# Kernel tuning notes

Hardware: AMD Instinct MI355X
Metric: run time of the kernel (lower is better)

The kernel has to match this reference:

```python
import jax, jax.numpy as jnp
import numpy as np
from jax.ops import segment_sum, segment_max

ALPHA = 0.01  # leaky relu slope

def _cmul(a, b):
    # complex multiply on last-axis (re, im) pairs
    re = a[..., 0] * b[..., 0] - a[..., 1] * b[..., 1]
    im = a[..., 0] * b[..., 1] + a[..., 1] * b[..., 0]
    return jnp.stack((re, im), axis=-1)

def setup_inputs() -> dict:
    key = jax.random.key(0)
    ks = jax.random.split(key, 8)
    N, D, M, E, L, H, R, FH = 50000, 64, 3, 100000, 4, 8, 5, 128
    return {
        "features": jax.random.normal(ks[0], (N, D), jnp.float32),
        "attn1_w": jax.random.normal(ks[1], (M, H, D), jnp.float32) * 0.1,
        "attn2":   jax.random.normal(ks[2], (M, H, D), jnp.float32) * 0.1,
        "r_vec":   jax.random.normal(ks[3], (R, D // 2, 2), jnp.float32),
        "proj_w1": jax.random.normal(ks[4], (FH, H * D), jnp.float32) * 0.05,
        "proj_b1": jnp.zeros((FH,), jnp.float32),
        "proj_w2": jax.random.normal(ks[5], (1, FH), jnp.float32) * 0.1,
        "inst":    jax.random.randint(ks[6], (M, E, L), 0, N),
        "etypes":  jax.random.randint(ks[7], (M, L - 1), 0, 2 * R, dtype=jnp.int32),
    }

def reference(features, attn1_w, attn2, r_vec, proj_w1, proj_b1, proj_w2, inst, etypes):
    N, D = features.shape
    M, E, L = inst.shape
    H = attn1_w.shape[1]
    # --- conjugate-augmented, L2-normalized relation rotations ([2R, D/2, 2]) ---
    rn = r_vec / jnp.linalg.norm(r_vec, axis=2, keepdims=True)
    conj = rn * jnp.array([1.0, -1.0], rn.dtype)
    r_full = jnp.stack((rn, conj), axis=1).reshape(2 * r_vec.shape[0], r_vec.shape[1], 2)

    node_embs = []  # per-metapath [N, H*D]
    for m in range(M):
        # SemanticEncoder: gather + rotation recurrence + mean over path positions
        edata = features[inst[m]]                       # [E, L, D]
        edc = edata.reshape(E, L, D // 2, 2)
        # final_r_vec: backward cumulative complex product; position L-1 = identity
        ident = jnp.concatenate(
            [jnp.ones((D // 2, 1), edata.dtype), jnp.zeros((D // 2, 1), edata.dtype)], axis=-1)
        fr = [None] * L
        fr[L - 1] = ident
        for i in range(L - 2, -1, -1):
            fr[i] = _cmul(fr[i + 1], r_full[etypes[m, i]])
        fr = jnp.stack(fr, axis=0)                      # [L, D/2, 2]
        rotated = _cmul(edc, fr[None])                  # [E, L, D/2, 2] (pos L-1 rotated by identity)
        me = rotated.reshape(E, L, D).mean(axis=1)      # metapath embedding [E, D]

        # MessageAggregator: GAT-style segment softmax over instances per dst node
        dst = inst[m, :, 0]                             # [E]
        a1 = features[dst] @ attn1_w[m].T               # [E, H]
        a2 = jnp.einsum('ed,hd->eh', me, attn2[m])      # [E, H]
        a = jax.nn.leaky_relu(a1 + a2, ALPHA)           # [E, H]
        amax = segment_max(a, dst, num_segments=N)      # [N, H]
        amax = jnp.where(jnp.isfinite(amax), amax, 0.0)
        ex = jnp.exp(a - amax[dst])                     # [E, H]
        den = segment_sum(ex, dst, num_segments=N)      # [N, H]
        attn = ex / jnp.where(den[dst] > 0, den[dst], 1.0)
        agg = segment_sum(attn[:, :, None] * me[:, None, :], dst, num_segments=N)  # [N, H, D]
        node_embs.append(jax.nn.elu(agg).reshape(N, H * D))

    # Subgraph_Fusion: semantic attention over metapaths
    z = jnp.stack(node_embs, axis=1)                    # [N, M, H*D]
    w = jnp.tanh(z @ proj_w1.T + proj_b1) @ proj_w2.T   # [N, M, 1]
    beta = jax.nn.softmax(w.mean(axis=0), axis=0)       # [M, 1]
    out = (beta[None] * z).sum(axis=1)                  # [N, H*D]
    return out
```

## Files before the change

kernel.cpp:

```cpp
#include <hip/hip_runtime.h>
#include <hip/hip_bf16.h>
#include <math.h>

#define NN 50000
#define DD 64
#define MM 3
#define EE 100000
#define LL 4
#define HH 8
#define FHH 128
#define HD 512
#define NROWS (NN*MM)
#define LRELU_ALPHA 0.01f

#define WSUM_BINS 256
#define WSUM_SZ (MM*WSUM_BINS)
#define BINS (MM*NN)
#define NBLK ((BINS + 1023)/1024)
#define GT_TILE 224

#define OFF_ZB    0
#define OFF_WSUM  (NROWS*HD/2)
#define OFF_BETA  (OFF_WSUM + WSUM_SZ)
#define OFF_W1BF  (OFF_BETA + 16)
#define OFF_WU    (OFF_W1BF + 32768)
#define OFF_GT    (OFF_WU + 6144)
#define OFF_INTS  (OFF_GT + MM*NN*32)
#define IOFF_CNT    0
#define IOFF_CURSOR (IOFF_CNT + BINS)
#define IOFF_PART   (IOFF_CURSOR + BINS)
#define IOFF_BSUM   (IOFF_PART + BINS)
#define IOFF_BTOP   (IOFF_BSUM + 256)
#define IOFF_ORDER  (IOFF_BTOP + 256)

typedef short v8s __attribute__((ext_vector_type(8)));
typedef float v4f __attribute__((ext_vector_type(4)));

__device__ __forceinline__ float elu_f(float x) {
    return x > 0.f ? x : (__expf(x) - 1.f);
}

__device__ __forceinline__ float tanh_fast(float x) {
    float e = __expf(2.f * x);
    return 1.f - 2.f / (e + 1.f);
}

__device__ __forceinline__ unsigned int pk_bf16x2(float x, float y) {
    float2 f2; f2.x = x; f2.y = y;
    __hip_bfloat162 h = __float22bfloat162_rn(f2);
    union { __hip_bfloat162 h; unsigned int u; } cv;
    cv.h = h;
    return cv.u;
}

__device__ __forceinline__ float bf_lo(unsigned int u) {
    union { unsigned int x; float f; } c; c.x = u << 16; return c.f;
}
__device__ __forceinline__ float bf_hi(unsigned int u) {
    union { unsigned int x; float f; } c; c.x = u & 0xffff0000u; return c.f;
}

__device__ __forceinline__ void build_frs(
    float frs[LL][DD/2][2], const float* r_vec, const int* etypes, int m, int t)
{
    if (t < DD/2) {
        float cr = 1.f, ci = 0.f;
        frs[LL-1][t][0] = 1.f; frs[LL-1][t][1] = 0.f;
        for (int i = LL-2; i >= 0; --i) {
            int et = etypes[m*(LL-1) + i];
            float rr = r_vec[((et>>1)*(DD/2) + t)*2 + 0];
            float ri = r_vec[((et>>1)*(DD/2) + t)*2 + 1];
            float inv = rsqrtf(rr*rr + ri*ri);
            rr *= inv; ri *= inv;
            if (et & 1) ri = -ri;
            float nr = cr*rr - ci*ri;
            float ni = cr*ri + ci*rr;
            cr = nr; ci = ni;
            frs[i][t][0] = cr; frs[i][t][1] = ci;
        }
    }
}


__global__ __launch_bounds__(256) void hist_kernel(
    const int* __restrict__ inst, int* __restrict__ cnt)
{
    int e = blockIdx.x*256 + threadIdx.x;
    int m = blockIdx.y;
    if (e >= EE) return;
    int dst = inst[((size_t)m*EE + e)*LL];
    atomicAdd(&cnt[m*NN + dst], 1);
}

__global__ __launch_bounds__(256) void scan_partial_kernel(
    const int* __restrict__ cnt, int* __restrict__ part, int* __restrict__ bsum)
{
    __shared__ int sd[256];
    const int t = threadIdx.x;
    const int base = blockIdx.x*1024 + t*4;
    int v0=0,v1=0,v2=0,v3=0;
    if (base+3 < BINS) {
        int4 v = *(const int4*)&cnt[base];
        v0=v.x; v1=v.y; v2=v.z; v3=v.w;
    } else {
        if (base+0 < BINS) v0 = cnt[base+0];
        if (base+1 < BINS) v1 = cnt[base+1];
        if (base+2 < BINS) v2 = cnt[base+2];
        if (base+3 < BINS) v3 = cnt[base+3];
    }
    int tot = v0+v1+v2+v3;
    sd[t] = tot; __syncthreads();
    #pragma unroll
    for (int off = 1; off < 256; off <<= 1) {
        int val = (t >= off) ? sd[t-off] : 0;
        __syncthreads();
        sd[t] += val;
        __syncthreads();
    }
    int excl = sd[t] - tot;
    if (base+0 < BINS) part[base+0] = excl;
    if (base+1 < BINS) part[base+1] = excl + v0;
    if (base+2 < BINS) part[base+2] = excl + v0 + v1;
    if (base+3 < BINS) part[base+3] = excl + v0 + v1 + v2;
    if (t == 255) bsum[blockIdx.x] = sd[255];
}

__global__ __launch_bounds__(256) void scan_tops_kernel(
    const int* __restrict__ bsum, int* __restrict__ btop)
{
    __shared__ int sd[256];
    const int t = threadIdx.x;
    int v = (t < NBLK) ? bsum[t] : 0;
    sd[t] = v; __syncthreads();
    #pragma unroll
    for (int off = 1; off < 256; off <<= 1) {
        int val = (t >= off) ? sd[t-off] : 0;
        __syncthreads();
        sd[t] += val;
        __syncthreads();
    }
    if (t < NBLK) btop[t] = sd[t] - v;
}

__global__ __launch_bounds__(256) void scatter_kernel(
    const int* __restrict__ inst, const int* __restrict__ part,
    const int* __restrict__ btop, int* __restrict__ cursor,
    int* __restrict__ order)
{
    int e = blockIdx.x*256 + threadIdx.x;
    int m = blockIdx.y;
    if (e >= EE) return;
    int dst = inst[((size_t)m*EE + e)*LL];
    int bin = m*NN + dst;
    int pos = part[bin] + btop[bin >> 10] + atomicAdd(&cursor[bin], 1);
    order[pos] = e;
}

__global__ __launch_bounds__(64) void ugen_kernel(
    const float* __restrict__ r_vec,
    const int* __restrict__ etypes,
    const float* __restrict__ attn1_w,
    const float* __restrict__ attn2,
    float* __restrict__ Wu)
{
    const int m = blockIdx.x;
    __shared__ float frs[LL][DD/2][2];
    const int t = threadIdx.x;
    build_frs(frs, r_vec, etypes, m, t);
    __syncthreads();
    for (int idx = t; idx < 32*64; idx += 64) {
        int j = idx >> 6, d = idx & 63, p = d >> 1;
        int l = (j < 8) ? 0 : (j >> 3);
        int h = j & 7;
        float fr = frs[l][p][0], fi = frs[l][p][1];
        float w2r = attn2[m*HD + h*DD + 2*p];
        float w2i = attn2[m*HD + h*DD + 2*p + 1];
        float u = (d & 1) ? (fr*w2i - fi*w2r) : (fr*w2r + fi*w2i);
        float val = 0.25f * u + ((j < 8) ? attn1_w[m*HD + h*DD + d] : 0.f);
        Wu[(m*32 + j)*64 + d] = val;
    }
}

__global__ __launch_bounds__(256) void gt_kernel(
    const float* __restrict__ features,
    const float* __restrict__ Wu,
    float* __restrict__ gt)
{
    __shared__ float xs[GT_TILE*65];
    const int m = blockIdx.y;
    const int node0 = blockIdx.x * GT_TILE;
    const int t = threadIdx.x;
    #pragma unroll
    for (int i = 0; i < 14; ++i) {
        int idx = t + 256*i;
        int r = idx >> 4, c4 = idx & 15;
        int gr = node0 + r;
        float4 v = make_float4(0.f,0.f,0.f,0.f);
        if (gr < NN) v = ((const float4*)features)[gr*16 + c4];
        float* dst = &xs[r*65 + c4*4];
        dst[0]=v.x; dst[1]=v.y; dst[2]=v.z; dst[3]=v.w;
    }
    __syncthreads();
    if (t >= GT_TILE) return;
    int node = node0 + t;
    float acc[32];
    #pragma unroll
    for (int j=0;j<32;++j) acc[j]=0.f;
    const float* Wm = Wu + m*2048;
    for (int d = 0; d < 64; ++d) {
        float x = xs[t*65 + d];
        #pragma unroll
        for (int j = 0; j < 32; ++j)
            acc[j] += x * Wm[j*64 + d];
    }
    if (node < NN) {
        float* o = gt + ((size_t)m*NN + node)*32;
        #pragma unroll
        for (int j4 = 0; j4 < 8; ++j4) {
            float4 v; v.x=acc[j4*4]; v.y=acc[j4*4+1]; v.z=acc[j4*4+2]; v.w=acc[j4*4+3];
            ((float4*)o)[j4] = v;
        }
    }
}

__global__ __launch_bounds__(256) void node_kernel(
    const float* __restrict__ features,
    const float* __restrict__ r_vec,
    const int*   __restrict__ etypes,
    const int*   __restrict__ inst,
    const int*   __restrict__ order,
    const int*   __restrict__ part,
    const int*   __restrict__ btop,
    const int*   __restrict__ cnt,
    const float* __restrict__ gt,
    ushort* __restrict__ Zb)
{
    const int m = blockIdx.y;
    __shared__ float frs[LL][DD/2][2];
    const int t = threadIdx.x;
    build_frs(frs, r_vec, etypes, m, t);
    __syncthreads();

    const int lane = t & 63;
    const int wid  = t >> 6;
    const int node = blockIdx.x*4 + wid;

    const int bin = m*NN + node;
    ushort* zrow = Zb + ((size_t)node*MM + m)*HD;
    const int ecnt = cnt[bin];
    if (ecnt == 0) {
        if (!(lane&1)) {
            #pragma unroll
            for (int h = 0; h < HH; ++h)
                ((unsigned int*)zrow)[h*32 + (lane>>1)] = 0u;
        }
        return;
    }
    const int start = part[bin] + btop[bin >> 10];

    const int p = lane >> 1;
    const float sgn = (lane & 1) ? 1.0f : -1.0f;
    float flx[LL], fly[LL];
    #pragma unroll
    for (int l = 0; l < LL; ++l) { flx[l] = frs[l][p][0]; fly[l] = frs[l][p][1]; }

    const float x0  = features[(size_t)node*DD + lane];
    const float pr0 = __shfl_xor(x0, 1);
    const float me0 = x0*flx[0] + sgn*pr0*fly[0];

    const float c0v = (lane < HH) ? gt[((size_t)bin)*32 + lane] : 0.f;
    const int lsel = lane >> 3;
    const int* instm = inst + (size_t)m*EE*LL;
    const float* gtm = gt + (size_t)m*NN*32;

    float acc[HH];
    #pragma unroll
    for (int h = 0; h < HH; ++h) acc[h] = 0.f;
    float den = 0.f;

    for (int q = 0; q < ecnt; ++q) {
        int e = order[start + q];
        const int* ip = instm + e*LL;
        int i1 = ip[1], i2 = ip[2], i3 = ip[3];

        int idxg = (lsel == 1) ? i1 : ((lsel == 2) ? i2 : i3);
        float gv = 0.f;
        if (lane >= 8 && lane < 32)
            gv = gtm[(size_t)idxg*32 + lane];
        gv += __shfl_xor(gv, 16);
        gv += __shfl_xor(gv, 8);

        float x1 = features[(size_t)i1*DD + lane];
        float x2 = features[(size_t)i2*DD + lane];
        float x3 = features[(size_t)i3*DD + lane];
        float me = me0;
        me += x1*flx[1] + sgn*__shfl_xor(x1,1)*fly[1];
        me += x2*flx[2] + sgn*__shfl_xor(x2,1)*fly[2];
        me += x3*flx[3] + sgn*__shfl_xor(x3,1)*fly[3];
        me *= 0.25f;

        float ex = 0.f;
        if (lane < HH) {
            float a = c0v + gv;
            a = a > 0.f ? a : LRELU_ALPHA*a;
            ex = __expf(a);
            den += ex;
        }
        #pragma unroll
        for (int h = 0; h < HH; ++h)
            acc[h] += __shfl(ex, h) * me;
    }

    #pragma unroll
    for (int h = 0; h < HH; ++h) {
        float dh = __shfl(den, h);
        float v = elu_f(acc[h] / dh);
        float vn = __shfl_xor(v, 1);
        if (!(lane&1))
            ((unsigned int*)zrow)[h*32 + (lane>>1)] = pk_bf16x2(v, vn);
    }
}


__global__ __launch_bounds__(64) void cvt_w1_kernel(
    const float* __restrict__ w1, ushort* __restrict__ w1bf)
{
    int i = blockIdx.x*64 + threadIdx.x;
    float4 v = ((const float4*)w1)[i];
    uint2 p;
    p.x = pk_bf16x2(v.x, v.y);
    p.y = pk_bf16x2(v.z, v.w);
    ((uint2*)w1bf)[i] = p;
}

__global__ __launch_bounds__(256,3) void wproj_kernel(
    const ushort* __restrict__ Zb,
    const ushort* __restrict__ w1bf,
    const float* __restrict__ b1,
    const float* __restrict__ w2,
    float* __restrict__ wsum)
{
    __shared__ ushort As[128*72];
    __shared__ ushort Bs[128*72];
    __shared__ float wacc[MM];
    const int t = threadIdx.x;
    const int row0 = blockIdx.x * 128;
    if (t < MM) wacc[t] = 0.f;
    const int lane = t & 63;
    const int wid  = t >> 6;
    const int ln   = lane & 15;
    const int quad = lane >> 4;
    const int wr   = wid >> 1;
    const int wc   = wid & 1;

    v4f acc[4][4];
    #pragma unroll
    for (int i=0;i<4;++i)
        #pragma unroll
        for (int j=0;j<4;++j)
            acc[i][j] = (v4f){0.f,0.f,0.f,0.f};

    const uint4* zb4 = (const uint4*)Zb;
    const uint4* wb4 = (const uint4*)w1bf;

    for (int kt = 0; kt < 8; ++kt) {
        __syncthreads();
        #pragma unroll
        for (int i = 0; i < 4; ++i) {
            int idx = t + 256*i;
            int r = idx >> 3, k8 = idx & 7;
            int gr = row0 + r;
            uint4 v = make_uint4(0u,0u,0u,0u);
            if (gr < NROWS) v = zb4[(size_t)gr*64 + kt*8 + k8];
            *(uint4*)&As[r*72 + k8*8] = v;
        }
        #pragma unroll
        for (int i = 0; i < 4; ++i) {
            int idx = t + 256*i;
            int f = idx >> 3, k8 = idx & 7;
            uint4 v = wb4[f*64 + kt*8 + k8];
            *(uint4*)&Bs[f*72 + k8*8] = v;
        }
        __syncthreads();
        #pragma unroll
        for (int kk = 0; kk < 2; ++kk) {
            v8s a[4], b[4];
            #pragma unroll
            for (int i=0;i<4;++i)
                a[i] = *(const v8s*)&As[(wr*64 + i*16 + ln)*72 + kk*32 + quad*8];
            #pragma unroll
            for (int j=0;j<4;++j)
                b[j] = *(const v8s*)&Bs[(wc*64 + j*16 + ln)*72 + kk*32 + quad*8];
            #pragma unroll
            for (int i=0;i<4;++i)
                #pragma unroll
                for (int j=0;j<4;++j)
                    acc[i][j] = __builtin_amdgcn_mfma_f32_16x16x32_bf16(
                        a[i], b[j], acc[i][j], 0, 0, 0);
        }
    }

    float b1v[4], w2v[4];
    #pragma unroll
    for (int j=0;j<4;++j) {
        int col = wc*64 + j*16 + ln;
        b1v[j] = b1[col];
        w2v[j] = w2[col];
    }
    #pragma unroll
    for (int i=0;i<4;++i) {
        #pragma unroll
        for (int reg=0;reg<4;++reg) {
            float s = 0.f;
            #pragma unroll
            for (int j=0;j<4;++j)
                s += tanh_fast(acc[i][j][reg] + b1v[j]) * w2v[j];
            s += __shfl_xor(s, 1);
            s += __shfl_xor(s, 2);
            s += __shfl_xor(s, 4);
            s += __shfl_xor(s, 8);
            int grow = row0 + wr*64 + i*16 + quad*4 + reg;
            if (ln == 0 && grow < NROWS)
                atomicAdd(&wacc[grow % MM], s);
        }
    }
    __syncthreads();
    if (t < MM)
        atomicAdd(&wsum[t*WSUM_BINS + (blockIdx.x & (WSUM_BINS-1))], wacc[t]);
}

__global__ void beta_kernel(const float* __restrict__ wsum, float* __restrict__ beta)
{
    __shared__ float sm[MM];
    int t = threadIdx.x;
    if (t < MM) {
        float s = 0.f;
        for (int i = 0; i < WSUM_BINS; ++i) s += wsum[t*WSUM_BINS + i];
        sm[t] = s / (float)NN;
    }
    __syncthreads();
    if (t < MM) {
        float a = sm[0], b = sm[1], c = sm[2];
        float mx = fmaxf(a, fmaxf(b, c));
        float e0 = __expf(a-mx), e1 = __expf(b-mx), e2 = __expf(c-mx);
        float tot = e0+e1+e2;
        float mine = (t==0?e0:(t==1?e1:e2));
        beta[t] = mine/tot;
    }
}

__global__ __launch_bounds__(256) void out_kernel(
    const ushort* __restrict__ Zb, const float* __restrict__ beta,
    float* __restrict__ out)
{
    int i = blockIdx.x*256 + threadIdx.x;
    int n  = i >> 6;
    int jj = i & 63;
    float b0 = beta[0], b1v = beta[1], b2 = beta[2];
    const uint4* zb4 = (const uint4*)Zb;
    uint4 v0 = zb4[((size_t)n*MM + 0)*64 + jj];
    uint4 v1 = zb4[((size_t)n*MM + 1)*64 + jj];
    uint4 v2 = zb4[((size_t)n*MM + 2)*64 + jj];
    float o[8];
    o[0] = b0*bf_lo(v0.x) + b1v*bf_lo(v1.x) + b2*bf_lo(v2.x);
    o[1] = b0*bf_hi(v0.x) + b1v*bf_hi(v1.x) + b2*bf_hi(v2.x);
    o[2] = b0*bf_lo(v0.y) + b1v*bf_lo(v1.y) + b2*bf_lo(v2.y);
    o[3] = b0*bf_hi(v0.y) + b1v*bf_hi(v1.y) + b2*bf_hi(v2.y);
    o[4] = b0*bf_lo(v0.z) + b1v*bf_lo(v1.z) + b2*bf_lo(v2.z);
    o[5] = b0*bf_hi(v0.z) + b1v*bf_hi(v1.z) + b2*bf_hi(v2.z);
    o[6] = b0*bf_lo(v0.w) + b1v*bf_lo(v1.w) + b2*bf_lo(v2.w);
    o[7] = b0*bf_hi(v0.w) + b1v*bf_hi(v1.w) + b2*bf_hi(v2.w);
    float4* op = (float4*)(out + (size_t)n*HD + jj*8);
    op[0] = make_float4(o[0],o[1],o[2],o[3]);
    op[1] = make_float4(o[4],o[5],o[6],o[7]);
}

extern "C" void kernel_launch(void* const* d_in, const int* in_sizes, int n_in,
                              void* d_out, int out_size, void* d_ws, size_t ws_size,
                              hipStream_t stream) {
    const float* features = (const float*)d_in[0];
    const float* attn1_w  = (const float*)d_in[1];
    const float* attn2    = (const float*)d_in[2];
    const float* r_vec    = (const float*)d_in[3];
    const float* proj_w1  = (const float*)d_in[4];
    const float* proj_b1  = (const float*)d_in[5];
    const float* proj_w2  = (const float*)d_in[6];
    const int*   inst     = (const int*)d_in[7];
    const int*   etypes   = (const int*)d_in[8];
    float* out = (float*)d_out;

    float* ws    = (float*)d_ws;
    ushort* Zb   = (ushort*)(ws + OFF_ZB);
    float* wsum  = ws + OFF_WSUM;
    float* beta  = ws + OFF_BETA;
    ushort* w1bf = (ushort*)(ws + OFF_W1BF);
    float* Wu    = ws + OFF_WU;
    float* gt    = ws + OFF_GT;
    int* ints    = (int*)(ws + OFF_INTS);
    int* cnt     = ints + IOFF_CNT;
    int* cursor  = ints + IOFF_CURSOR;
    int* part    = ints + IOFF_PART;
    int* bsum    = ints + IOFF_BSUM;
    int* btop    = ints + IOFF_BTOP;
    int* order   = ints + IOFF_ORDER;

    hipMemsetAsync(cnt, 0, (size_t)2*BINS*sizeof(int), stream);
    hipMemsetAsync(wsum, 0, (size_t)WSUM_SZ*sizeof(float), stream);

    cvt_w1_kernel<<<256, 64, 0, stream>>>(proj_w1, w1bf);
    ugen_kernel<<<MM, 64, 0, stream>>>(r_vec, etypes, attn1_w, attn2, Wu);
    gt_kernel<<<dim3((NN + GT_TILE-1)/GT_TILE, MM), 256, 0, stream>>>(features, Wu, gt);
    hist_kernel<<<dim3((EE+255)/256, MM), 256, 0, stream>>>(inst, cnt);
    scan_partial_kernel<<<NBLK, 256, 0, stream>>>(cnt, part, bsum);
    scan_tops_kernel<<<1, 256, 0, stream>>>(bsum, btop);
    scatter_kernel<<<dim3((EE+255)/256, MM), 256, 0, stream>>>(inst, part, btop, cursor, order);
    node_kernel<<<dim3(NN/4, MM), 256, 0, stream>>>(
        features, r_vec, etypes, inst, order, part, btop, cnt, gt, Zb);
    wproj_kernel<<<(NROWS + 127)/128, 256, 0, stream>>>(Zb, w1bf, proj_b1, proj_w2, wsum);
    beta_kernel<<<1, 64, 0, stream>>>(wsum, beta);
    out_kernel<<<NN*64/256, 256, 0, stream>>>(Zb, beta, out);
}
```

Measured before the change: 425.7 us.

## Gather fp16 features, pre-sort instance records, and unroll node edge loop by two

Adds a pass that converts features to fp16 so the node kernel's random row gathers move half the bytes. The scatter kernel now writes each instance's three path indices as an int4 record in sorted order, which removes the order-then-inst double indirection. The node kernel loads 64 records per wave and broadcasts them with readlane, then processes two edges per iteration to expose more memory-level parallelism. This adds an extra conversion kernel and fp16 rounding of the features, and it costs more registers.

```diff
diff --git a/kernel.cpp b/kernel.cpp
--- a/kernel.cpp
+++ b/kernel.cpp
@@ -1,5 +1,6 @@
 #include <hip/hip_runtime.h>
 #include <hip/hip_bf16.h>
+#include <hip/hip_fp16.h>
 #include <math.h>
 
 #define NN 50000
@@ -31,7 +32,9 @@
 #define IOFF_PART   (IOFF_CURSOR + BINS)
 #define IOFF_BSUM   (IOFF_PART + BINS)
 #define IOFF_BTOP   (IOFF_BSUM + 256)
-#define IOFF_ORDER  (IOFF_BTOP + 256)
+#define IOFF_REC    (IOFF_BTOP + 256)
+#define INTS_END    (IOFF_REC + 4*MM*EE)
+#define OFF_F16   (OFF_INTS + INTS_END)
 
 typedef short v8s __attribute__((ext_vector_type(8)));
 typedef float v4f __attribute__((ext_vector_type(4)));
@@ -81,6 +84,18 @@
     }
 }
 
+__global__ __launch_bounds__(256) void fcvt_kernel(
+    const float* __restrict__ f, ushort* __restrict__ f16)
+{
+    int i = blockIdx.x*256 + threadIdx.x;
+    float4 v = ((const float4*)f)[i];
+    __half2 h0 = __float22half2_rn(make_float2(v.x, v.y));
+    __half2 h1 = __float22half2_rn(make_float2(v.z, v.w));
+    union { __half2 h; unsigned int u; } c0, c1;
+    c0.h = h0; c1.h = h1;
+    ((uint2*)f16)[i] = make_uint2(c0.u, c1.u);
+}
+
 
 __global__ __launch_bounds__(256) void hist_kernel(
     const int* __restrict__ inst, int* __restrict__ cnt)
@@ -143,17 +158,17 @@
 }
 
 __global__ __launch_bounds__(256) void scatter_kernel(
-    const int* __restrict__ inst, const int* __restrict__ part,
+    const int4* __restrict__ inst4, const int* __restrict__ part,
     const int* __restrict__ btop, int* __restrict__ cursor,
-    int* __restrict__ order)
+    int4* __restrict__ rec)
 {
     int e = blockIdx.x*256 + threadIdx.x;
     int m = blockIdx.y;
     if (e >= EE) return;
-    int dst = inst[((size_t)m*EE + e)*LL];
-    int bin = m*NN + dst;
+    int4 v = inst4[(size_t)m*EE + e];
+    int bin = m*NN + v.x;
     int pos = part[bin] + btop[bin >> 10] + atomicAdd(&cursor[bin], 1);
-    order[pos] = e;
+    rec[pos] = make_int4(v.y, v.z, v.w, 0);
 }
 
 __global__ __launch_bounds__(64) void ugen_kernel(
@@ -224,11 +239,10 @@
 }
 
 __global__ __launch_bounds__(256) void node_kernel(
-    const float* __restrict__ features,
+    const ushort* __restrict__ f16,
     const float* __restrict__ r_vec,
     const int*   __restrict__ etypes,
-    const int*   __restrict__ inst,
-    const int*   __restrict__ order,
+    const int4*  __restrict__ rec4,
     const int*   __restrict__ part,
     const int*   __restrict__ btop,
     const int*   __restrict__ cnt,
@@ -264,13 +278,14 @@
     #pragma unroll
     for (int l = 0; l < LL; ++l) { flx[l] = frs[l][p][0]; fly[l] = frs[l][p][1]; }
 
-    const float x0  = features[(size_t)node*DD + lane];
+    const __half* fh = (const __half*)f16;
+    const float x0  = __half2float(fh[node*DD + lane]);
     const float pr0 = __shfl_xor(x0, 1);
     const float me0 = x0*flx[0] + sgn*pr0*fly[0];
 
     const float c0v = (lane < HH) ? gt[((size_t)bin)*32 + lane] : 0.f;
     const int lsel = lane >> 3;
-    const int* instm = inst + (size_t)m*EE*LL;
+    const bool gm = (lane >= 8 && lane < 32);
     const float* gtm = gt + (size_t)m*NN*32;
 
     float acc[HH];
@@ -278,43 +293,103 @@
     for (int h = 0; h < HH; ++h) acc[h] = 0.f;
     float den = 0.f;
 
-    for (int q = 0; q < ecnt; ++q) {
-        int e = order[start + q];
-        const int* ip = instm + e*LL;
-        int i1 = ip[1], i2 = ip[2], i3 = ip[3];
-
-        int idxg = (lsel == 1) ? i1 : ((lsel == 2) ? i2 : i3);
-        float gv = 0.f;
-        if (lane >= 8 && lane < 32)
-            gv = gtm[(size_t)idxg*32 + lane];
-        gv += __shfl_xor(gv, 16);
-        gv += __shfl_xor(gv, 8);
-
-        float x1 = features[(size_t)i1*DD + lane];
-        float x2 = features[(size_t)i2*DD + lane];
-        float x3 = features[(size_t)i3*DD + lane];
-        float me = me0;
-        me += x1*flx[1] + sgn*__shfl_xor(x1,1)*fly[1];
-        me += x2*flx[2] + sgn*__shfl_xor(x2,1)*fly[2];
-        me += x3*flx[3] + sgn*__shfl_xor(x3,1)*fly[3];
-        me *= 0.25f;
-
-        float ex = 0.f;
-        if (lane < HH) {
-            float a = c0v + gv;
-            a = a > 0.f ? a : LRELU_ALPHA*a;
-            ex = __expf(a);
-            den += ex;
-        }
-        #pragma unroll
-        for (int h = 0; h < HH; ++h)
-            acc[h] += __shfl(ex, h) * me;
+    for (int base = 0; base < ecnt; base += 64) {
+        int rem = ecnt - base; if (rem > 64) rem = 64;
+        int4 rec = make_int4(0,0,0,0);
+        if (lane < rem) rec = rec4[start + base + lane];
+
+        int q = 0;
+        for (; q + 2 <= rem; q += 2) {
+            int a1 = __builtin_amdgcn_readlane(rec.x, q);
+            int a2 = __builtin_amdgcn_readlane(rec.y, q);
+            int a3 = __builtin_amdgcn_readlane(rec.z, q);
+            int b1 = __builtin_amdgcn_readlane(rec.x, q+1);
+            int b2 = __builtin_amdgcn_readlane(rec.y, q+1);
+            int b3 = __builtin_amdgcn_readlane(rec.z, q+1);
+
+            int ia = (lsel == 1) ? a1 : ((lsel == 2) ? a2 : a3);
+            int ib = (lsel == 1) ? b1 : ((lsel == 2) ? b2 : b3);
+            float gva = 0.f, gvb = 0.f;
+            if (gm) {
+                gva = gtm[(size_t)ia*32 + lane];
+                gvb = gtm[(size_t)ib*32 + lane];
+            }
+            float xa1 = __half2float(fh[a1*DD + lane]);
+            float xa2 = __half2float(fh[a2*DD + lane]);
+            float xa3 = __half2float(fh[a3*DD + lane]);
+            float xb1 = __half2float(fh[b1*DD + lane]);
+            float xb2 = __half2float(fh[b2*DD + lane]);
+            float xb3 = __half2float(fh[b3*DD + lane]);
+
+            gva += __shfl_xor(gva, 16);
+            gva += __shfl_xor(gva, 8);
+            gvb += __shfl_xor(gvb, 16);
+            gvb += __shfl_xor(gvb, 8);
+
+            float mea = me0;
+            mea += xa1*flx[1] + sgn*__shfl_xor(xa1,1)*fly[1];
+            mea += xa2*flx[2] + sgn*__shfl_xor(xa2,1)*fly[2];
+            mea += xa3*flx[3] + sgn*__shfl_xor(xa3,1)*fly[3];
+            mea *= 0.25f;
+            float meb = me0;
+            meb += xb1*flx[1] + sgn*__shfl_xor(xb1,1)*fly[1];
+            meb += xb2*flx[2] + sgn*__shfl_xor(xb2,1)*fly[2];
+            meb += xb3*flx[3] + sgn*__shfl_xor(xb3,1)*fly[3];
+            meb *= 0.25f;
+
+            float exa = 0.f, exb = 0.f;
+            if (lane < HH) {
+                float aa = c0v + gva;
+                aa = aa > 0.f ? aa : LRELU_ALPHA*aa;
+                exa = __expf(aa);
+                float ab = c0v + gvb;
+                ab = ab > 0.f ? ab : LRELU_ALPHA*ab;
+                exb = __expf(ab);
+                den += exa + exb;
+            }
+            #pragma unroll
+            for (int h = 0; h < HH; ++h)
+                acc[h] += __shfl(exa, h)*mea + __shfl(exb, h)*meb;
+        }
+        if (q < rem) {
+            int a1 = __builtin_amdgcn_readlane(rec.x, q);
+            int a2 = __builtin_amdgcn_readlane(rec.y, q);
+            int a3 = __builtin_amdgcn_readlane(rec.z, q);
+
+            int ia = (lsel == 1) ? a1 : ((lsel == 2) ? a2 : a3);
+            float gva = 0.f;
+            if (gm) gva = gtm[(size_t)ia*32 + lane];
+            float xa1 = __half2float(fh[a1*DD + lane]);
+            float xa2 = __half2float(fh[a2*DD + lane]);
+            float xa3 = __half2float(fh[a3*DD + lane]);
+
+            gva += __shfl_xor(gva, 16);
+            gva += __shfl_xor(gva, 8);
+
+            float mea = me0;
+            mea += xa1*flx[1] + sgn*__shfl_xor(xa1,1)*fly[1];
+            mea += xa2*flx[2] + sgn*__shfl_xor(xa2,1)*fly[2];
+            mea += xa3*flx[3] + sgn*__shfl_xor(xa3,1)*fly[3];
+            mea *= 0.25f;
+
+            float exa = 0.f;
+            if (lane < HH) {
+                float aa = c0v + gva;
+                aa = aa > 0.f ? aa : LRELU_ALPHA*aa;
+                exa = __expf(aa);
+                den += exa;
+            }
+            #pragma unroll
+            for (int h = 0; h < HH; ++h)
+                acc[h] += __shfl(exa, h)*mea;
+        }
     }
 
     #pragma unroll
     for (int h = 0; h < HH; ++h) {
         float dh = __shfl(den, h);
-        float v = elu_f(acc[h] / dh);
+        float inv = __builtin_amdgcn_rcpf(dh);
+        float v = elu_f(acc[h] * inv);
         float vn = __shfl_xor(v, 1);
         if (!(lane&1))
             ((unsigned int*)zrow)[h*32 + (lane>>1)] = pk_bf16x2(v, vn);
@@ -502,20 +577,23 @@
     int* part    = ints + IOFF_PART;
     int* bsum    = ints + IOFF_BSUM;
     int* btop    = ints + IOFF_BTOP;
-    int* order   = ints + IOFF_ORDER;
+    int4* rec4   = (int4*)(ints + IOFF_REC);
+    ushort* f16  = (ushort*)(ws + OFF_F16);
 
     hipMemsetAsync(cnt, 0, (size_t)2*BINS*sizeof(int), stream);
     hipMemsetAsync(wsum, 0, (size_t)WSUM_SZ*sizeof(float), stream);
 
+    fcvt_kernel<<<NN*DD/4/256, 256, 0, stream>>>(features, f16);
     cvt_w1_kernel<<<256, 64, 0, stream>>>(proj_w1, w1bf);
     ugen_kernel<<<MM, 64, 0, stream>>>(r_vec, etypes, attn1_w, attn2, Wu);
     gt_kernel<<<dim3((NN + GT_TILE-1)/GT_TILE, MM), 256, 0, stream>>>(features, Wu, gt);
     hist_kernel<<<dim3((EE+255)/256, MM), 256, 0, stream>>>(inst, cnt);
     scan_partial_kernel<<<NBLK, 256, 0, stream>>>(cnt, part, bsum);
     scan_tops_kernel<<<1, 256, 0, stream>>>(bsum, btop);
-    scatter_kernel<<<dim3((EE+255)/256, MM), 256, 0, stream>>>(inst, part, btop, cursor, order);
+    scatter_kernel<<<dim3((EE+255)/256, MM), 256, 0, stream>>>(
+        (const int4*)inst, part, btop, cursor, rec4);
     node_kernel<<<dim3(NN/4, MM), 256, 0, stream>>>(
-        features, r_vec, etypes, inst, order, part, btop, cnt, gt, Zb);
+        f16, r_vec, etypes, rec4, part, btop, cnt, gt, Zb);
     wproj_kernel<<<(NROWS + 127)/128, 256, 0, stream>>>(Zb, w1bf, proj_b1, proj_w2, wsum);
     beta_kernel<<<1, 64, 0, stream>>>(wsum, beta);
     out_kernel<<<NN*64/256, 256, 0, stream>>>(Zb, beta, out);
```

Measured after the change: 409.6 us. 3.8% less time.

## Use fp16 feature copy, packed edge records, and two-edges-per-wave gather in node kernel

Applied to the files above, without the earlier changes.

Features are converted to an fp16 copy, so each node gather reads half the bytes. The scatter pass now writes the three non-destination indices of each instance as a packed int4 record, which removes the indirection through order and inst. Segment start and count are precomputed into an int2 array, and the rotation factors are precomputed once instead of rebuilt in every block. Each wave now handles two edges per iteration, one per 32-lane half, using complex pairs per lane, and the halves are merged with shuffles at the end. This adds fp16 precision loss in the message embedding and an extra conversion kernel and fixup kernel.

```diff
diff --git a/kernel.cpp b/kernel.cpp
--- a/kernel.cpp
+++ b/kernel.cpp
@@ -1,5 +1,6 @@
 #include <hip/hip_runtime.h>
 #include <hip/hip_bf16.h>
+#include <hip/hip_fp16.h>
 #include <math.h>
 
 #define NN 50000
@@ -24,14 +25,18 @@
 #define OFF_BETA  (OFF_WSUM + WSUM_SZ)
 #define OFF_W1BF  (OFF_BETA + 16)
 #define OFF_WU    (OFF_W1BF + 32768)
-#define OFF_GT    (OFF_WU + 6144)
+#define OFF_FRS   (OFF_WU + 6144)
+#define OFF_GT    (OFF_FRS + 768)
 #define OFF_INTS  (OFF_GT + MM*NN*32)
 #define IOFF_CNT    0
 #define IOFF_CURSOR (IOFF_CNT + BINS)
 #define IOFF_PART   (IOFF_CURSOR + BINS)
 #define IOFF_BSUM   (IOFF_PART + BINS)
 #define IOFF_BTOP   (IOFF_BSUM + 256)
-#define IOFF_ORDER  (IOFF_BTOP + 256)
+#define IOFF_SEGC   (IOFF_BTOP + 256)
+#define IOFF_REC    (IOFF_SEGC + 2*BINS)
+#define INTS_END    (IOFF_REC + 4*MM*EE)
+#define OFF_F16   (OFF_INTS + INTS_END)
 
 typedef short v8s __attribute__((ext_vector_type(8)));
 typedef float v4f __attribute__((ext_vector_type(4)));
@@ -58,6 +63,11 @@
 }
 __device__ __forceinline__ float bf_hi(unsigned int u) {
     union { unsigned int x; float f; } c; c.x = u & 0xffff0000u; return c.f;
+}
+
+__device__ __forceinline__ float2 h2f(unsigned int u) {
+    union { unsigned int x; __half2 h; } c; c.x = u;
+    return __half22float2(c.h);
 }
 
 __device__ __forceinline__ void build_frs(
@@ -81,6 +91,18 @@
     }
 }
 
+__global__ __launch_bounds__(256) void fcvt_kernel(
+    const float* __restrict__ f, ushort* __restrict__ f16)
+{
+    int i = blockIdx.x*256 + threadIdx.x;
+    float4 v = ((const float4*)f)[i];
+    __half2 h0 = __float22half2_rn(make_float2(v.x, v.y));
+    __half2 h1 = __float22half2_rn(make_float2(v.z, v.w));
+    union { __half2 h; unsigned int u; } c0, c1;
+    c0.h = h0; c1.h = h1;
+    ((uint2*)f16)[i] = make_uint2(c0.u, c1.u);
+}
+
 
 __global__ __launch_bounds__(256) void hist_kernel(
     const int* __restrict__ inst, int* __restrict__ cnt)
@@ -142,18 +164,28 @@
     if (t < NBLK) btop[t] = sd[t] - v;
 }
 
+__global__ __launch_bounds__(256) void fixup_kernel(
+    int* __restrict__ part, const int* __restrict__ btop,
+    const int* __restrict__ cnt, int2* __restrict__ segc)
+{
+    int i = blockIdx.x*256 + threadIdx.x;
+    if (i >= BINS) return;
+    int p = part[i] + btop[i >> 10];
+    part[i] = p;
+    segc[i] = make_int2(p, cnt[i]);
+}
+
 __global__ __launch_bounds__(256) void scatter_kernel(
-    const int* __restrict__ inst, const int* __restrict__ part,
-    const int* __restrict__ btop, int* __restrict__ cursor,
-    int* __restrict__ order)
+    const int4* __restrict__ inst4, const int* __restrict__ part,
+    int* __restrict__ cursor, int4* __restrict__ rec)
 {
     int e = blockIdx.x*256 + threadIdx.x;
     int m = blockIdx.y;
     if (e >= EE) return;
-    int dst = inst[((size_t)m*EE + e)*LL];
-    int bin = m*NN + dst;
-    int pos = part[bin] + btop[bin >> 10] + atomicAdd(&cursor[bin], 1);
-    order[pos] = e;
+    int4 v = inst4[(size_t)m*EE + e];
+    int bin = m*NN + v.x;
+    int pos = part[bin] + atomicAdd(&cursor[bin], 1);
+    rec[pos] = make_int4(v.y, v.z, v.w, 0);
 }
 
 __global__ __launch_bounds__(64) void ugen_kernel(
@@ -161,13 +193,23 @@
     const int* __restrict__ etypes,
     const float* __restrict__ attn1_w,
     const float* __restrict__ attn2,
-    float* __restrict__ Wu)
+    float* __restrict__ Wu,
+    float* __restrict__ frs_pk)
 {
     const int m = blockIdx.x;
     __shared__ float frs[LL][DD/2][2];
     const int t = threadIdx.x;
     build_frs(frs, r_vec, etypes, m, t);
     __syncthreads();
+    if (t < 32) {
+        float4 v0, v1;
+        v0.x = frs[0][t][0]; v0.y = frs[0][t][1];
+        v0.z = frs[1][t][0]; v0.w = frs[1][t][1];
+        v1.x = frs[2][t][0]; v1.y = frs[2][t][1];
+        v1.z = frs[3][t][0]; v1.w = frs[3][t][1];
+        ((float4*)frs_pk)[(m*32 + t)*2 + 0] = v0;
+        ((float4*)frs_pk)[(m*32 + t)*2 + 1] = v1;
+    }
     for (int idx = t; idx < 32*64; idx += 64) {
         int j = idx >> 6, d = idx & 63, p = d >> 1;
         int l = (j < 8) ? 0 : (j >> 3);
@@ -224,100 +266,105 @@
 }
 
 __global__ __launch_bounds__(256) void node_kernel(
-    const float* __restrict__ features,
-    const float* __restrict__ r_vec,
-    const int*   __restrict__ etypes,
-    const int*   __restrict__ inst,
-    const int*   __restrict__ order,
-    const int*   __restrict__ part,
-    const int*   __restrict__ btop,
-    const int*   __restrict__ cnt,
+    const unsigned int* __restrict__ f16u,
+    const float* __restrict__ frs_pk,
+    const int4*  __restrict__ rec4,
+    const int2*  __restrict__ segc,
     const float* __restrict__ gt,
     ushort* __restrict__ Zb)
 {
     const int m = blockIdx.y;
-    __shared__ float frs[LL][DD/2][2];
     const int t = threadIdx.x;
-    build_frs(frs, r_vec, etypes, m, t);
-    __syncthreads();
-
     const int lane = t & 63;
+    const int hl   = lane & 31;
+    const int half = lane >> 5;
     const int wid  = t >> 6;
     const int node = blockIdx.x*4 + wid;
 
     const int bin = m*NN + node;
     ushort* zrow = Zb + ((size_t)node*MM + m)*HD;
-    const int ecnt = cnt[bin];
+    const int2 sc = segc[bin];
+    const int start = sc.x, ecnt = sc.y;
     if (ecnt == 0) {
-        if (!(lane&1)) {
-            #pragma unroll
-            for (int h = 0; h < HH; ++h)
-                ((unsigned int*)zrow)[h*32 + (lane>>1)] = 0u;
-        }
+        ((uint4*)zrow)[lane] = make_uint4(0u,0u,0u,0u);
         return;
     }
-    const int start = part[bin] + btop[bin >> 10];
-
-    const int p = lane >> 1;
-    const float sgn = (lane & 1) ? 1.0f : -1.0f;
-    float flx[LL], fly[LL];
-    #pragma unroll
-    for (int l = 0; l < LL; ++l) { flx[l] = frs[l][p][0]; fly[l] = frs[l][p][1]; }
-
-    const float x0  = features[(size_t)node*DD + lane];
-    const float pr0 = __shfl_xor(x0, 1);
-    const float me0 = x0*flx[0] + sgn*pr0*fly[0];
-
-    const float c0v = (lane < HH) ? gt[((size_t)bin)*32 + lane] : 0.f;
-    const int lsel = lane >> 3;
-    const int* instm = inst + (size_t)m*EE*LL;
+
+    const float4* fp = (const float4*)frs_pk + ((size_t)m*32 + hl)*2;
+    const float4 fA = fp[0], fB = fp[1];
+    const float f0x=fA.x, f0y=fA.y, f1x=fA.z, f1y=fA.w;
+    const float f2x=fB.x, f2y=fB.y, f3x=fB.z, f3y=fB.w;
+
+    float2 x0 = h2f(f16u[(size_t)node*32 + hl]);
+    const float me0r = x0.x*f0x - x0.y*f0y;
+    const float me0i = x0.x*f0y + x0.y*f0x;
+
+    const float c0 = (hl < HH) ? gt[(size_t)bin*32 + hl] : 0.f;
+    const int lsel = hl >> 3;
+    const bool gm = (hl >= 8);
     const float* gtm = gt + (size_t)m*NN*32;
 
-    float acc[HH];
-    #pragma unroll
-    for (int h = 0; h < HH; ++h) acc[h] = 0.f;
+    float accr[HH], acci[HH];
+    #pragma unroll
+    for (int h = 0; h < HH; ++h) { accr[h] = 0.f; acci[h] = 0.f; }
     float den = 0.f;
 
-    for (int q = 0; q < ecnt; ++q) {
-        int e = order[start + q];
-        const int* ip = instm + e*LL;
-        int i1 = ip[1], i2 = ip[2], i3 = ip[3];
+    for (int q = 0; q < ecnt; q += 2) {
+        int myq = q + half;
+        bool valid = (myq < ecnt);
+        int qq = valid ? myq : (ecnt - 1);
+        int4 r = rec4[start + qq];
+        int i1 = r.x, i2 = r.y, i3 = r.z;
 
         int idxg = (lsel == 1) ? i1 : ((lsel == 2) ? i2 : i3);
         float gv = 0.f;
-        if (lane >= 8 && lane < 32)
-            gv = gtm[(size_t)idxg*32 + lane];
+        if (gm) gv = gtm[(size_t)idxg*32 + hl];
+
+        unsigned int u1 = f16u[(size_t)i1*32 + hl];
+        unsigned int u2 = f16u[(size_t)i2*32 + hl];
+        unsigned int u3 = f16u[(size_t)i3*32 + hl];
+
         gv += __shfl_xor(gv, 16);
         gv += __shfl_xor(gv, 8);
 
-        float x1 = features[(size_t)i1*DD + lane];
-        float x2 = features[(size_t)i2*DD + lane];
-        float x3 = features[(size_t)i3*DD + lane];
-        float me = me0;
-        me += x1*flx[1] + sgn*__shfl_xor(x1,1)*fly[1];
-        me += x2*flx[2] + sgn*__shfl_xor(x2,1)*fly[2];
-        me += x3*flx[3] + sgn*__shfl_xor(x3,1)*fly[3];
-        me *= 0.25f;
+        float2 x1 = h2f(u1), x2 = h2f(u2), x3 = h2f(u3);
+        float mer = me0r, mei = me0i;
+        mer += x1.x*f1x - x1.y*f1y;  mei += x1.x*f1y + x1.y*f1x;
+        mer += x2.x*f2x - x2.y*f2y;  mei += x2.x*f2y + x2.y*f2x;
+        mer += x3.x*f3x - x3.y*f3y;  mei += x3.x*f3y + x3.y*f3x;
+        mer *= 0.25f; mei *= 0.25f;
 
         float ex = 0.f;
-        if (lane < HH) {
-            float a = c0v + gv;
+        if (hl < HH) {
+            float a = c0 + gv;
             a = a > 0.f ? a : LRELU_ALPHA*a;
-            ex = __expf(a);
+            ex = valid ? __expf(a) : 0.f;
             den += ex;
         }
         #pragma unroll
-        for (int h = 0; h < HH; ++h)
-            acc[h] += __shfl(ex, h) * me;
+        for (int h = 0; h < HH; ++h) {
+            float e = __shfl(ex, (lane & 32) + h);
+            accr[h] += e * mer;
+            acci[h] += e * mei;
+        }
     }
 
     #pragma unroll
     for (int h = 0; h < HH; ++h) {
+        accr[h] += __shfl_xor(accr[h], 32);
+        acci[h] += __shfl_xor(acci[h], 32);
+    }
+    den += __shfl_xor(den, 32);
+
+    const int hbase = half ? 4 : 0;
+    #pragma unroll
+    for (int hh = 0; hh < 4; ++hh) {
+        int h = hbase + hh;
         float dh = __shfl(den, h);
-        float v = elu_f(acc[h] / dh);
-        float vn = __shfl_xor(v, 1);
-        if (!(lane&1))
-            ((unsigned int*)zrow)[h*32 + (lane>>1)] = pk_bf16x2(v, vn);
+        float inv = __builtin_amdgcn_rcpf(dh);
+        float vr = elu_f(accr[h] * inv);
+        float vi = elu_f(acci[h] * inv);
+        ((unsigned int*)zrow)[h*32 + hl] = pk_bf16x2(vr, vi);
     }
 }
 
@@ -495,6 +542,7 @@
     float* beta  = ws + OFF_BETA;
     ushort* w1bf = (ushort*)(ws + OFF_W1BF);
     float* Wu    = ws + OFF_WU;
+    float* frs_pk= ws + OFF_FRS;
     float* gt    = ws + OFF_GT;
     int* ints    = (int*)(ws + OFF_INTS);
     int* cnt     = ints + IOFF_CNT;
@@ -502,20 +550,25 @@
     int* part    = ints + IOFF_PART;
     int* bsum    = ints + IOFF_BSUM;
     int* btop    = ints + IOFF_BTOP;
-    int* order   = ints + IOFF_ORDER;
+    int2* segc   = (int2*)(ints + IOFF_SEGC);
+    int4* rec4   = (int4*)(ints + IOFF_REC);
+    ushort* f16  = (ushort*)(ws + OFF_F16);
 
     hipMemsetAsync(cnt, 0, (size_t)2*BINS*sizeof(int), stream);
     hipMemsetAsync(wsum, 0, (size_t)WSUM_SZ*sizeof(float), stream);
 
+    fcvt_kernel<<<NN*DD/4/256, 256, 0, stream>>>(features, f16);
     cvt_w1_kernel<<<256, 64, 0, stream>>>(proj_w1, w1bf);
-    ugen_kernel<<<MM, 64, 0, stream>>>(r_vec, etypes, attn1_w, attn2, Wu);
+    ugen_kernel<<<MM, 64, 0, stream>>>(r_vec, etypes, attn1_w, attn2, Wu, frs_pk);
     gt_kernel<<<dim3((NN + GT_TILE-1)/GT_TILE, MM), 256, 0, stream>>>(features, Wu, gt);
     hist_kernel<<<dim3((EE+255)/256, MM), 256, 0, stream>>>(inst, cnt);
     scan_partial_kernel<<<NBLK, 256, 0, stream>>>(cnt, part, bsum);
     scan_tops_kernel<<<1, 256, 0, stream>>>(bsum, btop);
-    scatter_kernel<<<dim3((EE+255)/256, MM), 256, 0, stream>>>(inst, part, btop, cursor, order);
+    fixup_kernel<<<(BINS+255)/256, 256, 0, stream>>>(part, btop, cnt, segc);
+    scatter_kernel<<<dim3((EE+255)/256, MM), 256, 0, stream>>>(
+        (const int4*)inst, part, cursor, rec4);
     node_kernel<<<dim3(NN/4, MM), 256, 0, stream>>>(
-        features, r_vec, etypes, inst, order, part, btop, cnt, gt, Zb);
+        (const unsigned int*)f16, frs_pk, rec4, segc, gt, Zb);
     wproj_kernel<<<(NROWS + 127)/128, 256, 0, stream>>>(Zb, w1bf, proj_b1, proj_w2, wsum);
     beta_kernel<<<1, 64, 0, stream>>>(wsum, beta);
     out_kernel<<<NN*64/256, 256, 0, stream>>>(Zb, beta, out);
```

Result: faster. 382.9 us (-10.1%).
